# Performance work log

Hardware: AMD Instinct MI355X
Metric: run time of the kernel (lower is better)

The kernel has to match this reference:

```python
import jax, jax.numpy as jnp
import numpy as np


def setup_inputs() -> dict:
    key = jax.random.key(0)
    k1, k2, k3, k4 = jax.random.split(key, 4)
    B, S, E, H = 8, 2048, 1024, 64
    x = jax.random.normal(k1, (B, S, E), dtype=jnp.float32)
    # nn.Linear(E, H, bias=False) weight is (H, E); we store transposed (E, H)
    scale = 1.0 / np.sqrt(E)
    Wk = jax.random.normal(k2, (E, H), dtype=jnp.float32) * scale
    Wq = jax.random.normal(k3, (E, H), dtype=jnp.float32) * scale
    Wv = jax.random.normal(k4, (E, H), dtype=jnp.float32) * scale
    return {"x": x, "Wk": Wk, "Wq": Wq, "Wv": Wv}


def reference(x, Wk, Wq, Wv):
    # x: (B, S, E); projections: (B, S, H)
    k = x @ Wk
    q = x @ Wq
    v = x @ Wv
    H = k.shape[-1]
    # scores: (B, S, S) with 1/sqrt(H) scaling as in the torch code
    scores = jnp.einsum("bqh,bkh->bqk", q, k) * (H ** -0.5)
    S = x.shape[1]
    causal = jnp.triu(jnp.full((S, S), -jnp.inf, dtype=scores.dtype), k=1)
    wei = jax.nn.softmax(scores + causal, axis=-1)
    # dropout p=0.0 -> identity
    return jnp.einsum("bqk,bkh->bqh", wei, v)
```

## Files before the change

### kernel.cpp

```cpp
#include <hip/hip_runtime.h>
#include <hip/hip_bf16.h>

typedef unsigned short ushort_t;
typedef __attribute__((ext_vector_type(8))) short short8;
typedef __attribute__((ext_vector_type(4))) float f32x4;

__device__ __forceinline__ float bf2f(ushort_t u) {
    unsigned int x = ((unsigned int)u) << 16;
    float f; __builtin_memcpy(&f, &x, 4); return f;
}
__device__ __forceinline__ ushort_t f2bf(float f) {
    unsigned int x; __builtin_memcpy(&x, &f, 4);
    x += 0x7fff + ((x >> 16) & 1);
    return (ushort_t)(x >> 16);
}

constexpr int E  = 1024;
constexpr int Hd = 64;
constexpr int S  = 2048;
constexpr int ROWS = 8 * 2048;
constexpr int NTOT = 192;
constexpr int LST  = 88;

__global__ __launch_bounds__(256)
void prep_wt(const float* __restrict__ Wk, const float* __restrict__ Wq,
             const float* __restrict__ Wv, ushort_t* __restrict__ WT)
{
    int idx = blockIdx.x * 256 + threadIdx.x;
    int n = idx >> 10;
    int kk = idx & 1023;
    const float* W = (n < 64) ? Wq : ((n < 128) ? Wk : Wv);
    int h = n & 63;
    WT[idx] = f2bf(W[kk * Hd + h]);
}

__global__ __launch_bounds__(256)
void proj_v7(const float* __restrict__ x, const ushort_t* __restrict__ WT,
             ushort_t* __restrict__ qo, ushort_t* __restrict__ ko,
             ushort_t* __restrict__ vTo)
{
    __shared__ alignas(16) ushort_t XS[32][LST];

    const int t    = threadIdx.x;
    const int w    = t >> 6;
    const int lane = t & 63;
    const int m    = lane & 15;
    const int g    = lane >> 4;
    const int rb   = blockIdx.x * 32;

    f32x4 accq[2], acck[2], accv[2];
    #pragma unroll
    for (int j = 0; j < 2; ++j) {
        accq[j] = (f32x4){0.f, 0.f, 0.f, 0.f};
        acck[j] = (f32x4){0.f, 0.f, 0.f, 0.f};
        accv[j] = (f32x4){0.f, 0.f, 0.f, 0.f};
    }

    const float* xptr = x + (size_t)(rb + (t >> 3)) * E + (t & 7) * 8;
    const ushort_t* wqp = WT + (size_t)(w * 16 + m) * E + g * 8;
    const ushort_t* wkp = wqp + (size_t)64 * E;
    const ushort_t* wvp = wqp + (size_t)128 * E;

    float4 xp0, xp1;
    short8 pbq[2], pbk[2], pbv[2], cbq[2], cbk[2], cbv[2];

    xp0 = *(const float4*)xptr;
    xp1 = *(const float4*)(xptr + 4);
    #pragma unroll
    for (int kt = 0; kt < 2; ++kt) {
        pbq[kt] = *(const short8*)(wqp + kt * 32);
        pbk[kt] = *(const short8*)(wkp + kt * 32);
        pbv[kt] = *(const short8*)(wvp + kt * 32);
    }

    #pragma unroll 1
    for (int c = 0; c < 16; ++c) {
        {
            short8 s;
            s[0]=(short)f2bf(xp0.x); s[1]=(short)f2bf(xp0.y);
            s[2]=(short)f2bf(xp0.z); s[3]=(short)f2bf(xp0.w);
            s[4]=(short)f2bf(xp1.x); s[5]=(short)f2bf(xp1.y);
            s[6]=(short)f2bf(xp1.z); s[7]=(short)f2bf(xp1.w);
            *(short8*)&XS[t >> 3][(t & 7) * 8] = s;
        }
        #pragma unroll
        for (int kt = 0; kt < 2; ++kt) {
            cbq[kt] = pbq[kt]; cbk[kt] = pbk[kt]; cbv[kt] = pbv[kt];
        }
        __syncthreads();

        if (c < 15) {
            const int k0 = (c + 1) * 64;
            xp0 = *(const float4*)(xptr + k0);
            xp1 = *(const float4*)(xptr + k0 + 4);
            #pragma unroll
            for (int kt = 0; kt < 2; ++kt) {
                pbq[kt] = *(const short8*)(wqp + k0 + kt * 32);
                pbk[kt] = *(const short8*)(wkp + k0 + kt * 32);
                pbv[kt] = *(const short8*)(wvp + k0 + kt * 32);
            }
        }

        #pragma unroll
        for (int kt = 0; kt < 2; ++kt) {
            short8 a0 = *(const short8*)&XS[m][kt * 32 + g * 8];
            short8 a1 = *(const short8*)&XS[16 + m][kt * 32 + g * 8];
            accq[0] = __builtin_amdgcn_mfma_f32_16x16x32_bf16(a0, cbq[kt], accq[0], 0, 0, 0);
            accq[1] = __builtin_amdgcn_mfma_f32_16x16x32_bf16(a1, cbq[kt], accq[1], 0, 0, 0);
            acck[0] = __builtin_amdgcn_mfma_f32_16x16x32_bf16(a0, cbk[kt], acck[0], 0, 0, 0);
            acck[1] = __builtin_amdgcn_mfma_f32_16x16x32_bf16(a1, cbk[kt], acck[1], 0, 0, 0);
            accv[0] = __builtin_amdgcn_mfma_f32_16x16x32_bf16(cbv[kt], a0, accv[0], 0, 0, 0);
            accv[1] = __builtin_amdgcn_mfma_f32_16x16x32_bf16(cbv[kt], a1, accv[1], 0, 0, 0);
        }
        __syncthreads();
    }

    const int col   = w * 16 + m;
    const int batch = rb >> 11;
    const int seq0  = rb & (S - 1);
    #pragma unroll
    for (int mt = 0; mt < 2; ++mt) {
        const int orow = rb + mt * 16 + g * 4;
        #pragma unroll
        for (int r = 0; r < 4; ++r) {
            qo[(size_t)(orow + r) * Hd + col] = f2bf(accq[mt][r] * 0.125f);
            ko[(size_t)(orow + r) * Hd + col] = f2bf(acck[mt][r]);
        }
    }
    #pragma unroll
    for (int ns = 0; ns < 2; ++ns)
        #pragma unroll
        for (int r = 0; r < 4; ++r) {
            const int h = w * 16 + g * 4 + r;
            vTo[(size_t)batch * Hd * S + (size_t)h * S + seq0 + ns * 16 + m]
                = f2bf(accv[ns][r]);
        }
}

__global__ __launch_bounds__(256)
void attn_part(const ushort_t* __restrict__ q, const ushort_t* __restrict__ k,
               const ushort_t* __restrict__ vT,
               float* __restrict__ lp, ushort_t* __restrict__ op)
{
    const int bi     = blockIdx.x;
    const int parity = bi & 3;
    const int pr     = bi >> 2;
    const int batch  = pr & 7;
    const int tile   = 31 - (pr >> 3);
    const int qs0    = tile * 64;
    const int sidx   = (batch * 32 + tile) * 4 + parity;

    const ushort_t* kb  = k  + (size_t)batch * S * Hd;
    const ushort_t* vTb = vT + (size_t)batch * Hd * S;

    const int t    = threadIdx.x;
    const int w    = t >> 6;
    const int lane = t & 63;
    const int m    = lane & 15;
    const int g    = lane >> 4;

    __shared__ alignas(16) ushort_t KS [64][LST];
    __shared__ alignas(16) ushort_t VTS[64][LST];
    __shared__ alignas(16) ushort_t PL[4][16][LST];

    const ushort_t* qrow = q + (size_t)(batch * S + qs0 + w * 16 + m) * Hd;
    short8 qf0 = *(const short8*)(qrow + g * 8);
    short8 qf1 = *(const short8*)(qrow + 32 + g * 8);

    f32x4 o[4];
    #pragma unroll
    for (int j = 0; j < 4; ++j) o[j] = (f32x4){0.f, 0.f, 0.f, 0.f};
    float lrun[4] = {0.f, 0.f, 0.f, 0.f};

    const int r1 = t >> 3, c16 = (t & 7) * 8;
    uint4 pk0, pk1, pv0, pv1;

    int c = parity;
    if (c <= tile) {
        const int key0 = c * 64;
        const ushort_t* kt_base = kb + (size_t)key0 * Hd;
        pk0 = *(const uint4*)(kt_base + t * 8);
        pk1 = *(const uint4*)(kt_base + (t + 256) * 8);
        pv0 = *(const uint4*)(vTb + (size_t)r1 * S + key0 + c16);
        pv1 = *(const uint4*)(vTb + (size_t)(r1 + 32) * S + key0 + c16);
    }

    for (; c <= tile; c += 4) {
        *(uint4*)&KS [r1][c16]       = pk0;
        *(uint4*)&KS [r1 + 32][c16]  = pk1;
        *(uint4*)&VTS[r1][c16]       = pv0;
        *(uint4*)&VTS[r1 + 32][c16]  = pv1;
        __syncthreads();

        if (c + 4 <= tile) {
            const int key0n = (c + 4) * 64;
            const ushort_t* kt_base = kb + (size_t)key0n * Hd;
            pk0 = *(const uint4*)(kt_base + t * 8);
            pk1 = *(const uint4*)(kt_base + (t + 256) * 8);
            pv0 = *(const uint4*)(vTb + (size_t)r1 * S + key0n + c16);
            pv1 = *(const uint4*)(vTb + (size_t)(r1 + 32) * S + key0n + c16);
        }

        f32x4 sacc[4];
        #pragma unroll
        for (int j = 0; j < 4; ++j) sacc[j] = (f32x4){0.f, 0.f, 0.f, 0.f};
        #pragma unroll
        for (int nt = 0; nt < 4; ++nt) {
            short8 b0 = *(const short8*)&KS[nt * 16 + m][g * 8];
            short8 b1 = *(const short8*)&KS[nt * 16 + m][32 + g * 8];
            sacc[nt] = __builtin_amdgcn_mfma_f32_16x16x32_bf16(qf0, b0, sacc[nt], 0, 0, 0);
            sacc[nt] = __builtin_amdgcn_mfma_f32_16x16x32_bf16(qf1, b1, sacc[nt], 0, 0, 0);
        }

        if (c == tile) {
            const int rowl = w * 16 + g * 4;
            #pragma unroll
            for (int nt = 0; nt < 4; ++nt) {
                const int keyl = nt * 16 + m;
                #pragma unroll
                for (int r = 0; r < 4; ++r)
                    sacc[nt][r] = (keyl > rowl + r) ? 0.f : __expf(sacc[nt][r]);
            }
        } else {
            #pragma unroll
            for (int nt = 0; nt < 4; ++nt)
                #pragma unroll
                for (int r = 0; r < 4; ++r)
                    sacc[nt][r] = __expf(sacc[nt][r]);
        }

        #pragma unroll
        for (int r = 0; r < 4; ++r)
            lrun[r] += (sacc[0][r] + sacc[1][r]) + (sacc[2][r] + sacc[3][r]);

        #pragma unroll
        for (int nt = 0; nt < 4; ++nt)
            #pragma unroll
            for (int r = 0; r < 4; ++r)
                PL[w][g * 4 + r][nt * 16 + m] = f2bf(sacc[nt][r]);

        short8 pa0 = *(const short8*)&PL[w][m][g * 8];
        short8 pa1 = *(const short8*)&PL[w][m][32 + g * 8];

        #pragma unroll
        for (int nt = 0; nt < 4; ++nt) {
            short8 vb0 = *(const short8*)&VTS[nt * 16 + m][g * 8];
            short8 vb1 = *(const short8*)&VTS[nt * 16 + m][32 + g * 8];
            o[nt] = __builtin_amdgcn_mfma_f32_16x16x32_bf16(pa0, vb0, o[nt], 0, 0, 0);
            o[nt] = __builtin_amdgcn_mfma_f32_16x16x32_bf16(pa1, vb1, o[nt], 0, 0, 0);
        }
        __syncthreads();
    }

    #pragma unroll
    for (int r = 0; r < 4; ++r) {
        float ts = lrun[r];
        #pragma unroll
        for (int d = 1; d < 16; d <<= 1) ts += __shfl_xor(ts, d, 64);
        if (m == 0) lp[sidx * 64 + w * 16 + g * 4 + r] = ts;
    }
    #pragma unroll
    for (int nt = 0; nt < 4; ++nt)
        #pragma unroll
        for (int r = 0; r < 4; ++r)
            op[(size_t)sidx * 4096 + (w * 16 + g * 4 + r) * 64 + nt * 16 + m]
                = f2bf(o[nt][r]);
}

__global__ __launch_bounds__(256)
void attn_merge(const float* __restrict__ lp, const ushort_t* __restrict__ op,
                float* __restrict__ out)
{
    const int bq    = blockIdx.x;
    const int batch = bq >> 5;
    const int tile  = bq & 31;
    const int s0    = (batch * 32 + tile) * 4;

    const int t   = threadIdx.x;
    const int row = t >> 2;
    const int c16 = (t & 3) * 16;

    float l = 0.f;
    #pragma unroll
    for (int p = 0; p < 4; ++p) l += lp[(s0 + p) * 64 + row];
    const float inv = 1.f / l;

    float acc[16];
    #pragma unroll
    for (int j = 0; j < 16; ++j) acc[j] = 0.f;
    #pragma unroll
    for (int p = 0; p < 4; ++p) {
        short8 a0 = *(const short8*)(op + (size_t)(s0 + p) * 4096 + row * 64 + c16);
        short8 a1 = *(const short8*)(op + (size_t)(s0 + p) * 4096 + row * 64 + c16 + 8);
        #pragma unroll
        for (int j = 0; j < 8; ++j) {
            acc[j]     += bf2f((ushort_t)a0[j]);
            acc[j + 8] += bf2f((ushort_t)a1[j]);
        }
    }
    float* dst = out + (size_t)(batch * S + tile * 64 + row) * Hd + c16;
    #pragma unroll
    for (int j = 0; j < 16; ++j) dst[j] = acc[j] * inv;
}

extern "C" void kernel_launch(void* const* d_in, const int* in_sizes, int n_in,
                              void* d_out, int out_size, void* d_ws, size_t ws_size,
                              hipStream_t stream) {
    const float* x  = (const float*)d_in[0];
    const float* Wk = (const float*)d_in[1];
    const float* Wq = (const float*)d_in[2];
    const float* Wv = (const float*)d_in[3];
    float* out = (float*)d_out;

    ushort_t* qws  = (ushort_t*)d_ws;
    ushort_t* kws  = qws + (size_t)ROWS * Hd;
    ushort_t* vTws = kws + (size_t)ROWS * Hd;
    ushort_t* WT   = vTws + (size_t)ROWS * Hd;
    float*    lpp  = (float*)(WT + (size_t)NTOT * E);
    ushort_t* opp  = (ushort_t*)(lpp + 1024 * 64);

    prep_wt<<<(NTOT * E) / 256, 256, 0, stream>>>(Wk, Wq, Wv, WT);
    proj_v7<<<ROWS / 32, 256, 0, stream>>>(x, WT, qws, kws, vTws);
    attn_part<<<1024, 256, 0, stream>>>(qws, kws, vTws, lpp, opp);
    attn_merge<<<256, 256, 0, stream>>>(lpp, opp, out);
}
```

Measured before the change: 135.8 us.

## Keep softmax probabilities in registers by computing transposed scores

The QK^T MFMA operands are swapped so each lane holds the transposed score tile. In that layout the exponentiated probabilities already match the A-operand layout of the 16x16x16 bf16 MFMA, so they are packed and fed straight into the PV product. This removes the per-tile LDS write and read of P and its shared buffer, and the row-sum reduction shrinks to two shuffles. The bf16 conversion also now uses the HIP intrinsic with pairwise packing, which changes the instruction mix. The trade-off is twice as many smaller PV MFMAs with narrower V loads from LDS.

```diff
diff --git a/kernel.cpp b/kernel.cpp
--- a/kernel.cpp
+++ b/kernel.cpp
@@ -3,6 +3,7 @@
 
 typedef unsigned short ushort_t;
 typedef __attribute__((ext_vector_type(8))) short short8;
+typedef __attribute__((ext_vector_type(4))) short short4v;
 typedef __attribute__((ext_vector_type(4))) float f32x4;
 
 __device__ __forceinline__ float bf2f(ushort_t u) {
@@ -10,9 +11,11 @@
     float f; __builtin_memcpy(&f, &x, 4); return f;
 }
 __device__ __forceinline__ ushort_t f2bf(float f) {
-    unsigned int x; __builtin_memcpy(&x, &f, 4);
-    x += 0x7fff + ((x >> 16) & 1);
-    return (ushort_t)(x >> 16);
+    __hip_bfloat16 h = __float2bfloat16(f);
+    ushort_t u; __builtin_memcpy(&u, &h, 2); return u;
+}
+__device__ __forceinline__ unsigned packbf2(float a, float b) {
+    return (unsigned)f2bf(a) | ((unsigned)f2bf(b) << 16);
 }
 
 constexpr int E  = 1024;
@@ -76,12 +79,12 @@
     #pragma unroll 1
     for (int c = 0; c < 16; ++c) {
         {
-            short8 s;
-            s[0]=(short)f2bf(xp0.x); s[1]=(short)f2bf(xp0.y);
-            s[2]=(short)f2bf(xp0.z); s[3]=(short)f2bf(xp0.w);
-            s[4]=(short)f2bf(xp1.x); s[5]=(short)f2bf(xp1.y);
-            s[6]=(short)f2bf(xp1.z); s[7]=(short)f2bf(xp1.w);
-            *(short8*)&XS[t >> 3][(t & 7) * 8] = s;
+            uint4 sv;
+            sv.x = packbf2(xp0.x, xp0.y);
+            sv.y = packbf2(xp0.z, xp0.w);
+            sv.z = packbf2(xp1.x, xp1.y);
+            sv.w = packbf2(xp1.z, xp1.w);
+            *(uint4*)&XS[t >> 3][(t & 7) * 8] = sv;
         }
         #pragma unroll
         for (int kt = 0; kt < 2; ++kt) {
@@ -161,7 +164,6 @@
 
     __shared__ alignas(16) ushort_t KS [64][LST];
     __shared__ alignas(16) ushort_t VTS[64][LST];
-    __shared__ alignas(16) ushort_t PL[4][16][LST];
 
     const ushort_t* qrow = q + (size_t)(batch * S + qs0 + w * 16 + m) * Hd;
     short8 qf0 = *(const short8*)(qrow + g * 8);
@@ -170,7 +172,8 @@
     f32x4 o[4];
     #pragma unroll
     for (int j = 0; j < 4; ++j) o[j] = (f32x4){0.f, 0.f, 0.f, 0.f};
-    float lrun[4] = {0.f, 0.f, 0.f, 0.f};
+    float lrun = 0.f;
+    const int qr = w * 16 + m;
 
     const int r1 = t >> 3, c16 = (t & 7) * 8;
     uint4 pk0, pk1, pv0, pv1;
@@ -208,19 +211,18 @@
         for (int nt = 0; nt < 4; ++nt) {
             short8 b0 = *(const short8*)&KS[nt * 16 + m][g * 8];
             short8 b1 = *(const short8*)&KS[nt * 16 + m][32 + g * 8];
-            sacc[nt] = __builtin_amdgcn_mfma_f32_16x16x32_bf16(qf0, b0, sacc[nt], 0, 0, 0);
-            sacc[nt] = __builtin_amdgcn_mfma_f32_16x16x32_bf16(qf1, b1, sacc[nt], 0, 0, 0);
+            sacc[nt] = __builtin_amdgcn_mfma_f32_16x16x32_bf16(b0, qf0, sacc[nt], 0, 0, 0);
+            sacc[nt] = __builtin_amdgcn_mfma_f32_16x16x32_bf16(b1, qf1, sacc[nt], 0, 0, 0);
         }
 
         if (c == tile) {
-            const int rowl = w * 16 + g * 4;
             #pragma unroll
-            for (int nt = 0; nt < 4; ++nt) {
-                const int keyl = nt * 16 + m;
+            for (int nt = 0; nt < 4; ++nt)
                 #pragma unroll
-                for (int r = 0; r < 4; ++r)
-                    sacc[nt][r] = (keyl > rowl + r) ? 0.f : __expf(sacc[nt][r]);
-            }
+                for (int r = 0; r < 4; ++r) {
+                    const int keyl = nt * 16 + g * 4 + r;
+                    sacc[nt][r] = (keyl > qr) ? 0.f : __expf(sacc[nt][r]);
+                }
         } else {
             #pragma unroll
             for (int nt = 0; nt < 4; ++nt)
@@ -230,34 +232,34 @@
         }
 
         #pragma unroll
-        for (int r = 0; r < 4; ++r)
-            lrun[r] += (sacc[0][r] + sacc[1][r]) + (sacc[2][r] + sacc[3][r]);
-
-        #pragma unroll
         for (int nt = 0; nt < 4; ++nt)
+            lrun += (sacc[nt][0] + sacc[nt][1]) + (sacc[nt][2] + sacc[nt][3]);
+
+        unsigned pw0[4], pw1[4];
+        #pragma unroll
+        for (int s = 0; s < 4; ++s) {
+            pw0[s] = packbf2(sacc[s][0], sacc[s][1]);
+            pw1[s] = packbf2(sacc[s][2], sacc[s][3]);
+        }
+
+        #pragma unroll
+        for (int s = 0; s < 4; ++s) {
+            short4v pa;
+            { unsigned u2[2] = {pw0[s], pw1[s]}; __builtin_memcpy(&pa, u2, 8); }
             #pragma unroll
-            for (int r = 0; r < 4; ++r)
-                PL[w][g * 4 + r][nt * 16 + m] = f2bf(sacc[nt][r]);
-
-        short8 pa0 = *(const short8*)&PL[w][m][g * 8];
-        short8 pa1 = *(const short8*)&PL[w][m][32 + g * 8];
-
-        #pragma unroll
-        for (int nt = 0; nt < 4; ++nt) {
-            short8 vb0 = *(const short8*)&VTS[nt * 16 + m][g * 8];
-            short8 vb1 = *(const short8*)&VTS[nt * 16 + m][32 + g * 8];
-            o[nt] = __builtin_amdgcn_mfma_f32_16x16x32_bf16(pa0, vb0, o[nt], 0, 0, 0);
-            o[nt] = __builtin_amdgcn_mfma_f32_16x16x32_bf16(pa1, vb1, o[nt], 0, 0, 0);
+            for (int nt = 0; nt < 4; ++nt) {
+                short4v vb = *(const short4v*)&VTS[nt * 16 + m][s * 16 + g * 4];
+                o[nt] = __builtin_amdgcn_mfma_f32_16x16x16bf16_1k(pa, vb, o[nt], 0, 0, 0);
+            }
         }
         __syncthreads();
     }
 
-    #pragma unroll
-    for (int r = 0; r < 4; ++r) {
-        float ts = lrun[r];
-        #pragma unroll
-        for (int d = 1; d < 16; d <<= 1) ts += __shfl_xor(ts, d, 64);
-        if (m == 0) lp[sidx * 64 + w * 16 + g * 4 + r] = ts;
+    {
+        float ts = lrun;
+        ts += __shfl_xor(ts, 16, 64);
+        ts += __shfl_xor(ts, 32, 64);
+        if (lane < 16) lp[sidx * 64 + w * 16 + m] = ts;
     }
     #pragma unroll
     for (int nt = 0; nt < 4; ++nt)
```

Measured after the change: 133.5 us. No clear change (-1.7%).
